# Performance work log

Hardware: AMD Instinct MI355X
Metric: run time of the kernel (lower is better)

## Reference

```python
import jax, jax.numpy as jnp
import numpy as np

B, C, H, W = 16, 4, 64, 64
D_MODEL, D_INNER, D_STATE, D_CONV, DT_RANK = 64, 128, 16, 4, 4


def _mamba_params(key, prefix):
    ks = jax.random.split(key, 6)
    s = lambda k, shape, scale: jax.random.normal(k, shape, jnp.float32) * scale
    return {
        prefix + 'in_proj_w': s(ks[0], (2 * D_INNER, D_MODEL), 0.05),
        prefix + 'conv_w': s(ks[1], (D_INNER, 1, D_CONV), 0.2),
        prefix + 'conv_b': jnp.zeros((D_INNER,), jnp.float32),
        prefix + 'x_proj_w': s(ks[2], (DT_RANK + 2 * D_STATE, D_INNER), 0.05),
        prefix + 'dt_proj_w': s(ks[3], (D_INNER, DT_RANK), 0.1),
        prefix + 'dt_proj_b': s(ks[4], (D_INNER,), 0.1),
        prefix + 'A_log': jnp.log(jnp.broadcast_to(jnp.arange(1, D_STATE + 1, dtype=jnp.float32), (D_INNER, D_STATE))),
        prefix + 'D': jnp.ones((D_INNER,), jnp.float32),
        prefix + 'out_proj_w': s(ks[5], (D_MODEL, D_INNER), 0.05),
    }


def setup_inputs() -> dict:
    key = jax.random.key(0)
    ks = jax.random.split(key, 5)
    inp = {'z_damaged': jax.random.normal(ks[0], (B, C, H, W), jnp.float32)}
    inp['emb_w'] = jax.random.normal(ks[1], (D_MODEL, C), jnp.float32) * 0.1
    inp['emb_b'] = jnp.zeros((D_MODEL,), jnp.float32)
    inp.update(_mamba_params(ks[2], 'm1_'))
    inp.update(_mamba_params(ks[3], 'm2_'))
    inp['ln1_g'] = jnp.ones((D_MODEL,), jnp.float32)
    inp['ln1_b'] = jnp.zeros((D_MODEL,), jnp.float32)
    inp['ln2_g'] = jnp.ones((D_MODEL,), jnp.float32)
    inp['ln2_b'] = jnp.zeros((D_MODEL,), jnp.float32)
    inp['head_w'] = jax.random.normal(ks[4], (C, D_MODEL), jnp.float32) * 0.1
    inp['head_b'] = jnp.zeros((C,), jnp.float32)
    return inp


def _silu(x):
    return x * jax.nn.sigmoid(x)


def _layernorm(x, g, b, eps=1e-5):
    mu = x.mean(-1, keepdims=True)
    var = ((x - mu) ** 2).mean(-1, keepdims=True)
    return (x - mu) * jax.lax.rsqrt(var + eps) * g + b


def _mamba(x, in_proj_w, conv_w, conv_b, x_proj_w, dt_proj_w, dt_proj_b, A_log, Dp, out_proj_w):
    Bb, L, _ = x.shape
    xz = x @ in_proj_w.T                      # [B,L,2*Di]
    u, z = jnp.split(xz, 2, axis=-1)
    # causal depthwise conv over the sequence axis (left-pad K-1)
    uc = jnp.transpose(u, (0, 2, 1))          # [B,Di,L]
    uc = jax.lax.conv_general_dilated(uc, conv_w, (1,), [(D_CONV - 1, 0)],
                                      dimension_numbers=('NCH', 'OIH', 'NCH'),
                                      feature_group_count=D_INNER)
    uc = uc + conv_b[None, :, None]
    u = _silu(jnp.transpose(uc, (0, 2, 1)))   # [B,L,Di]
    x_dbl = u @ x_proj_w.T                    # [B,L,dt_rank+2N]
    dt, Bm, Cm = jnp.split(x_dbl, [DT_RANK, DT_RANK + D_STATE], axis=-1)
    dt = jax.nn.softplus(dt @ dt_proj_w.T + dt_proj_b)   # [B,L,Di]
    A = -jnp.exp(A_log)                       # [Di,N]
    dA = jnp.exp(jnp.einsum('bld,dn->bldn', dt, A))      # [B,L,Di,N]
    dBu = jnp.einsum('bld,bln,bld->bldn', dt, Bm, u)     # [B,L,Di,N]

    def step(h, inp):
        dA_t, dBu_t, C_t = inp
        h = dA_t * h + dBu_t                  # [B,Di,N]
        return h, jnp.einsum('bdn,bn->bd', h, C_t)

    h0 = jnp.zeros((Bb, D_INNER, D_STATE), x.dtype)
    _, ys = jax.lax.scan(step, h0, (jnp.moveaxis(dA, 1, 0), jnp.moveaxis(dBu, 1, 0), jnp.moveaxis(Cm, 1, 0)))
    y = jnp.moveaxis(ys, 0, 1) + u * Dp       # [B,L,Di]
    y = y * _silu(z)
    return y @ out_proj_w.T                   # [B,L,D_MODEL]


def reference(z_damaged, emb_w, emb_b,
              m1_in_proj_w, m1_conv_w, m1_conv_b, m1_x_proj_w, m1_dt_proj_w, m1_dt_proj_b, m1_A_log, m1_D, m1_out_proj_w,
              m2_in_proj_w, m2_conv_w, m2_conv_b, m2_x_proj_w, m2_dt_proj_w, m2_dt_proj_b, m2_A_log, m2_D, m2_out_proj_w,
              ln1_g, ln1_b, ln2_g, ln2_b, head_w, head_b):
    Bz, Cz, Hh, Ww = z_damaged.shape
    zf = jnp.transpose(z_damaged, (0, 2, 3, 1)).reshape(Bz, Hh * Ww, Cz)
    feat = zf @ emb_w.T + emb_b
    feat = _mamba(feat, m1_in_proj_w, m1_conv_w, m1_conv_b, m1_x_proj_w, m1_dt_proj_w, m1_dt_proj_b, m1_A_log, m1_D, m1_out_proj_w)
    feat = _layernorm(feat, ln1_g, ln1_b)
    feat = _mamba(feat, m2_in_proj_w, m2_conv_w, m2_conv_b, m2_x_proj_w, m2_dt_proj_w, m2_dt_proj_b, m2_A_log, m2_D, m2_out_proj_w)
    feat = _layernorm(feat, ln2_g, ln2_b)
    drift = feat @ head_w.T + head_b          # [B,L,C]
    drift = jnp.transpose(drift.reshape(Bz, Hh, Ww, Cz), (0, 3, 1, 2))
    return z_damaged - drift
```

## Files before the change

kernel.cpp:

```cpp
#include <hip/hip_runtime.h>
#include <hip/hip_bf16.h>

#define DEV __device__ __forceinline__

static constexpr int Bn = 16;
static constexpr int Cc = 4;
static constexpr int HW = 4096;
static constexpr int BL = Bn * HW;
static constexpr int DM = 64;
static constexpr int DI = 128;
static constexpr int NS = 16;
static constexpr int NC = 256;
static constexpr int CS = HW / NC;

DEV float sigmoid_f(float x) { return 1.f / (1.f + __expf(-x)); }
DEV float softplus_f(float x) {
    return fmaxf(x, 0.f) + __logf(1.f + __expf(-fabsf(x)));
}
DEV float silu_f(float x) { return x / (1.f + __expf(-x)); }

__global__ __launch_bounds__(256) void k_embed(const float* __restrict__ z,
                                               const float* __restrict__ ew,
                                               const float* __restrict__ eb,
                                               float* __restrict__ feat) {
    int idx = blockIdx.x * 256 + threadIdx.x;
    if (idx >= BL * DM) return;
    int m = idx & 63;
    int bl = idx >> 6;
    int b = bl >> 12;
    int hw = bl & 4095;
    const float* zp = z + (size_t)b * Cc * HW + hw;
    float acc = eb[m];
#pragma unroll
    for (int c = 0; c < 4; ++c) acc += zp[(size_t)c * HW] * ew[m * 4 + c];
    feat[idx] = acc;
}

template <int K, int BN, int TN, int TM>
__global__ __launch_bounds__(256) void k_gemm(const float* __restrict__ in,
                                              const float* __restrict__ W,
                                              float* __restrict__ out,
                                              int Nfull) {
    constexpr int BM = 64;
    constexpr int CT = BN / TN;
    constexpr int RT = BM / TM;
    constexpr int KP = K + 4;
    constexpr int WP = BN + 4;
    __shared__ float As[BM * KP];
    __shared__ float Ws[K * WP];
    int tid = threadIdx.x;
    int n0 = blockIdx.y * BN;
    int row0 = blockIdx.x * BM;
    for (int i = tid; i < BN * (K / 4); i += 256) {
        int c = i / (K / 4);
        int k4 = i - c * (K / 4);
        float4 w = *reinterpret_cast<const float4*>(&W[(size_t)(n0 + c) * K + k4 * 4]);
        Ws[(k4 * 4 + 0) * WP + c] = w.x;
        Ws[(k4 * 4 + 1) * WP + c] = w.y;
        Ws[(k4 * 4 + 2) * WP + c] = w.z;
        Ws[(k4 * 4 + 3) * WP + c] = w.w;
    }
    for (int i = tid; i < BM * (K / 4); i += 256) {
        int r = i / (K / 4);
        int k4 = i - r * (K / 4);
        *reinterpret_cast<float4*>(&As[r * KP + k4 * 4]) =
            *reinterpret_cast<const float4*>(&in[(size_t)(row0 + r) * K + k4 * 4]);
    }
    __syncthreads();
    if (tid < CT * RT) {
        int ty = tid / CT, tx = tid - (tid / CT) * CT;
        int r0 = ty * TM, c0 = tx * TN;
        float acc[TM][TN];
#pragma unroll
        for (int i = 0; i < TM; ++i)
#pragma unroll
            for (int c = 0; c < TN; ++c) acc[i][c] = 0.f;
        for (int k = 0; k < K; k += 4) {
            float4 a[TM];
#pragma unroll
            for (int i = 0; i < TM; ++i)
                a[i] = *reinterpret_cast<const float4*>(&As[(r0 + i) * KP + k]);
            float bv[4][TN];
#pragma unroll
            for (int j = 0; j < 4; ++j)
#pragma unroll
                for (int c = 0; c < TN; ++c) bv[j][c] = Ws[(k + j) * WP + c0 + c];
#pragma unroll
            for (int i = 0; i < TM; ++i)
#pragma unroll
                for (int c = 0; c < TN; ++c)
                    acc[i][c] += a[i].x * bv[0][c] + a[i].y * bv[1][c]
                               + a[i].z * bv[2][c] + a[i].w * bv[3][c];
        }
#pragma unroll
        for (int i = 0; i < TM; ++i) {
            size_t o = (size_t)(row0 + r0 + i) * Nfull + n0 + c0;
            if constexpr (TN == 4) {
                float4 v = {acc[i][0], acc[i][1], acc[i][2], acc[i][3]};
                *reinterpret_cast<float4*>(&out[o]) = v;
            } else {
#pragma unroll
                for (int c = 0; c < TN; ++c) out[o + c] = acc[i][c];
            }
        }
    }
}

__global__ __launch_bounds__(256) void k_xproj(const float* __restrict__ xz,
                                               const float* __restrict__ W,
                                               const float* __restrict__ cw,
                                               const float* __restrict__ cb,
                                               float* __restrict__ xdbl) {
    constexpr int BM = 64, K = 128, BN = 36, TN = 3, TM = 4;
    constexpr int CT = BN / TN;
    constexpr int RT = BM / TM;
    constexpr int KP = K + 4;
    constexpr int WP = BN + 4;
    __shared__ float Xs[(BM + 3) * KP];
    __shared__ float Ws[K * WP];
    int tid = threadIdx.x;
    int row0 = blockIdx.x * BM;
    bool first = (row0 & 4095) == 0;
    for (int i = tid; i < BN * (K / 4); i += 256) {
        int c = i / (K / 4);
        int k4 = i - c * (K / 4);
        float4 w = *reinterpret_cast<const float4*>(&W[(size_t)c * K + k4 * 4]);
        Ws[(k4 * 4 + 0) * WP + c] = w.x;
        Ws[(k4 * 4 + 1) * WP + c] = w.y;
        Ws[(k4 * 4 + 2) * WP + c] = w.z;
        Ws[(k4 * 4 + 3) * WP + c] = w.w;
    }
    for (int i = tid; i < (BM + 3) * (K / 4); i += 256) {
        int r = i / (K / 4);
        int k4 = i - r * (K / 4);
        float4 v = {0, 0, 0, 0};
        if (!first || r >= 3)
            v = *reinterpret_cast<const float4*>(&xz[(size_t)(row0 - 3 + r) * 256 + k4 * 4]);
        *reinterpret_cast<float4*>(&Xs[r * KP + k4 * 4]) = v;
    }
    __syncthreads();
    {
        int rg = tid >> 5;
        int c0 = (tid & 31) * 4;
        float4 wr[4];
#pragma unroll
        for (int j = 0; j < 4; ++j)
            wr[j] = *reinterpret_cast<const float4*>(&cw[(c0 + j) * 4]);
        float4 cb4 = *reinterpret_cast<const float4*>(&cb[c0]);
        int R0 = rg * 8;
        float4 xr[11];
#pragma unroll
        for (int j = 0; j < 11; ++j)
            xr[j] = *reinterpret_cast<const float4*>(&Xs[(R0 + j) * KP + c0]);
        float4 ur[8];
#pragma unroll
        for (int j = 0; j < 8; ++j) {
            float4 acc;
            acc.x = cb4.x + wr[0].x * xr[j].x + wr[0].y * xr[j + 1].x + wr[0].z * xr[j + 2].x + wr[0].w * xr[j + 3].x;
            acc.y = cb4.y + wr[1].x * xr[j].y + wr[1].y * xr[j + 1].y + wr[1].z * xr[j + 2].y + wr[1].w * xr[j + 3].y;
            acc.z = cb4.z + wr[2].x * xr[j].z + wr[2].y * xr[j + 1].z + wr[2].z * xr[j + 2].z + wr[2].w * xr[j + 3].z;
            acc.w = cb4.w + wr[3].x * xr[j].w + wr[3].y * xr[j + 1].w + wr[3].z * xr[j + 2].w + wr[3].w * xr[j + 3].w;
            ur[j].x = silu_f(acc.x);
            ur[j].y = silu_f(acc.y);
            ur[j].z = silu_f(acc.z);
            ur[j].w = silu_f(acc.w);
        }
        __syncthreads();
#pragma unroll
        for (int j = 0; j < 8; ++j)
            *reinterpret_cast<float4*>(&Xs[(R0 + j) * KP + c0]) = ur[j];
    }
    __syncthreads();
    if (tid < CT * RT) {
        int ty = tid / CT, tx = tid - (tid / CT) * CT;
        int r0 = ty * TM, c0 = tx * TN;
        float acc[TM][TN];
#pragma unroll
        for (int i = 0; i < TM; ++i)
#pragma unroll
            for (int c = 0; c < TN; ++c) acc[i][c] = 0.f;
        for (int k = 0; k < K; k += 4) {
            float4 a[TM];
#pragma unroll
            for (int i = 0; i < TM; ++i)
                a[i] = *reinterpret_cast<const float4*>(&Xs[(r0 + i) * KP + k]);
            float bv[4][TN];
#pragma unroll
            for (int j = 0; j < 4; ++j)
#pragma unroll
                for (int c = 0; c < TN; ++c) bv[j][c] = Ws[(k + j) * WP + c0 + c];
#pragma unroll
            for (int i = 0; i < TM; ++i)
#pragma unroll
                for (int c = 0; c < TN; ++c)
                    acc[i][c] += a[i].x * bv[0][c] + a[i].y * bv[1][c]
                               + a[i].z * bv[2][c] + a[i].w * bv[3][c];
        }
#pragma unroll
        for (int i = 0; i < TM; ++i) {
            size_t o = (size_t)(row0 + r0 + i) * BN + c0;
#pragma unroll
            for (int c = 0; c < TN; ++c) xdbl[o + c] = acc[i][c];
        }
    }
}

DEV bool load_a_struct(const float* Alog, int d, float4& a0v, float4& a1v,
                       float4& a2v, float4& a3v, float& a0) {
    const float4* al = reinterpret_cast<const float4*>(Alog + d * NS);
    float4 t0 = al[0], t1 = al[1], t2 = al[2], t3 = al[3];
    a0v.x = -__expf(t0.x); a0v.y = -__expf(t0.y); a0v.z = -__expf(t0.z); a0v.w = -__expf(t0.w);
    a1v.x = -__expf(t1.x); a1v.y = -__expf(t1.y); a1v.z = -__expf(t1.z); a1v.w = -__expf(t1.w);
    a2v.x = -__expf(t2.x); a2v.y = -__expf(t2.y); a2v.z = -__expf(t2.z); a2v.w = -__expf(t2.w);
    a3v.x = -__expf(t3.x); a3v.y = -__expf(t3.y); a3v.z = -__expf(t3.z); a3v.w = -__expf(t3.w);
    a0 = a0v.x;
    float aa[16] = {a0v.x, a0v.y, a0v.z, a0v.w, a1v.x, a1v.y, a1v.z, a1v.w,
                    a2v.x, a2v.y, a2v.z, a2v.w, a3v.x, a3v.y, a3v.z, a3v.w};
    bool fast = true;
#pragma unroll
    for (int n = 0; n < 16; ++n)
        fast = fast && (fabsf(aa[n] - a0 * (float)(n + 1)) <= 1e-4f * (float)(n + 1));
    return fast;
}

#define POWERS(dt, a0, D0, D1, D2, D3)                        \
    {                                                         \
        float E1 = __expf((dt) * (a0));                       \
        float E2 = E1 * E1, E3 = E2 * E1, E4 = E2 * E2;       \
        float E5 = E3 * E2, E6 = E3 * E3, E7 = E4 * E3;       \
        float E8 = E4 * E4, E9 = E5 * E4, E10 = E5 * E5;      \
        float E11 = E6 * E5, E12 = E6 * E6, E13 = E7 * E6;    \
        float E14 = E7 * E7, E15 = E8 * E7, E16 = E8 * E8;    \
        D0 = {E1, E2, E3, E4};                                \
        D1 = {E5, E6, E7, E8};                                \
        D2 = {E9, E10, E11, E12};                             \
        D3 = {E13, E14, E15, E16};                            \
    }

#define UPD4D(H, DA, BV)                          \
    H.x = DA.x * H.x + du * BV.x;                 \
    H.y = DA.y * H.y + du * BV.y;                 \
    H.z = DA.z * H.z + du * BV.z;                 \
    H.w = DA.w * H.w + du * BV.w;

#define UPD4E(H, A, BV)                                  \
    H.x = __expf(dt * A.x) * H.x + du * BV.x;            \
    H.y = __expf(dt * A.y) * H.y + du * BV.y;            \
    H.z = __expf(dt * A.z) * H.z + du * BV.z;            \
    H.w = __expf(dt * A.w) * H.w + du * BV.w;

#define CONV_WARMUP                                                     \
    float x3 = 0.f, x2 = 0.f, x1 = 0.f;                                 \
    if (c != 0) {                                                       \
        size_t wb = ((size_t)b * HW + t0) * 256 + d;                    \
        x3 = xz[wb - 3 * 256];                                          \
        x2 = xz[wb - 2 * 256];                                          \
        x1 = xz[wb - 1 * 256];                                          \
    }

#define CONV_STEP(base)                                                 \
    float xv = xz[(base) * 256 + d];                                    \
    float cacc = cbv + cwv.x * x3 + cwv.y * x2 + cwv.z * x1 + cwv.w * xv; \
    float uu = cacc * sigmoid_f(cacc);                                  \
    x3 = x2; x2 = x1; x1 = xv;

__global__ __launch_bounds__(128, 4) void k_scan1(const float* __restrict__ xz,
                                                  const float* __restrict__ xdbl,
                                                  const float* __restrict__ dpw,
                                                  const float* __restrict__ dpb,
                                                  const float* __restrict__ Alog,
                                                  const float* __restrict__ cw,
                                                  const float* __restrict__ cb,
                                                  float* __restrict__ cS,
                                                  float* __restrict__ cDT) {
    int blk = blockIdx.x;
    int b = blk / NC;
    int c = blk % NC;
    int d = threadIdx.x;
    float4 a0v, a1v, a2v, a3v;
    float a0;
    bool fast = load_a_struct(Alog, d, a0v, a1v, a2v, a3v, a0);
    float4 w = *reinterpret_cast<const float4*>(dpw + d * 4);
    float bb = dpb[d];
    float4 cwv = *reinterpret_cast<const float4*>(cw + d * 4);
    float cbv = cb[d];
    float4 h0 = {0, 0, 0, 0}, h1 = {0, 0, 0, 0}, h2 = {0, 0, 0, 0}, h3 = {0, 0, 0, 0};
    float sdt = 0.f;
    int t0 = c * CS;
    CONV_WARMUP
    if (fast) {
        for (int tt = 0; tt < CS; ++tt) {
            size_t base = (size_t)b * HW + t0 + tt;
            const float4* xd4 = reinterpret_cast<const float4*>(xdbl + base * 36);
            float4 x0 = xd4[0];
            float4 B0 = xd4[1], B1 = xd4[2], B2 = xd4[3], B3 = xd4[4];
            float dt = softplus_f(w.x * x0.x + w.y * x0.y + w.z * x0.z + w.w * x0.w + bb);
            CONV_STEP(base)
            float du = dt * uu;
            sdt += dt;
            float4 D0, D1, D2, D3;
            POWERS(dt, a0, D0, D1, D2, D3)
            UPD4D(h0, D0, B0) UPD4D(h1, D1, B1) UPD4D(h2, D2, B2) UPD4D(h3, D3, B3)
        }
    } else {
        for (int tt = 0; tt < CS; ++tt) {
            size_t base = (size_t)b * HW + t0 + tt;
            const float4* xd4 = reinterpret_cast<const float4*>(xdbl + base * 36);
            float4 x0 = xd4[0];
            float4 B0 = xd4[1], B1 = xd4[2], B2 = xd4[3], B3 = xd4[4];
            float dt = softplus_f(w.x * x0.x + w.y * x0.y + w.z * x0.z + w.w * x0.w + bb);
            CONV_STEP(base)
            float du = dt * uu;
            sdt += dt;
            UPD4E(h0, a0v, B0) UPD4E(h1, a1v, B1) UPD4E(h2, a2v, B2) UPD4E(h3, a3v, B3)
        }
    }
    size_t o = (size_t)blk * DI + d;
    cDT[o] = sdt;
    float4* cs4 = reinterpret_cast<float4*>(cS + o * NS);
    cs4[0] = h0; cs4[1] = h1; cs4[2] = h2; cs4[3] = h3;
}

__global__ __launch_bounds__(256) void k_scan2(float* __restrict__ cS,
                                               const float* __restrict__ cDT,
                                               const float* __restrict__ Alog) {
    int idx = blockIdx.x * 256 + threadIdx.x;
    if (idx >= Bn * DI * NS) return;
    int n = idx & 15;
    int d = (idx >> 4) & 127;
    int b = idx >> 11;
    float a = -__expf(Alog[d * NS + n]);
    float h = 0.f;
    for (int c = 0; c < NC; ++c) {
        size_t o = (size_t)(b * NC + c) * DI + d;
        float s = cS[o * NS + n];
        cS[o * NS + n] = h;
        h = __expf(a * cDT[o]) * h + s;
    }
}

__global__ __launch_bounds__(128, 4) void k_scan3(float* __restrict__ uy,
                                                  const float* __restrict__ xz,
                                                  const float* __restrict__ xdbl,
                                                  const float* __restrict__ dpw,
                                                  const float* __restrict__ dpb,
                                                  const float* __restrict__ Alog,
                                                  const float* __restrict__ Dp,
                                                  const float* __restrict__ cw,
                                                  const float* __restrict__ cb,
                                                  const float* __restrict__ iS) {
    int blk = blockIdx.x;
    int b = blk / NC;
    int c = blk % NC;
    int d = threadIdx.x;
    float4 a0v, a1v, a2v, a3v;
    float a0;
    bool fast = load_a_struct(Alog, d, a0v, a1v, a2v, a3v, a0);
    float4 w = *reinterpret_cast<const float4*>(dpw + d * 4);
    float bb = dpb[d];
    float Dv = Dp[d];
    float4 cwv = *reinterpret_cast<const float4*>(cw + d * 4);
    float cbv = cb[d];
    size_t so = (size_t)blk * DI + d;
    const float4* is4 = reinterpret_cast<const float4*>(iS + so * NS);
    float4 h0 = is4[0], h1 = is4[1], h2 = is4[2], h3 = is4[3];
    int t0 = c * CS;
    CONV_WARMUP
    if (fast) {
        for (int tt = 0; tt < CS; ++tt) {
            size_t base = (size_t)b * HW + t0 + tt;
            const float4* xd4 = reinterpret_cast<const float4*>(xdbl + base * 36);
            float4 x0 = xd4[0];
            float4 B0 = xd4[1], B1 = xd4[2], B2 = xd4[3], B3 = xd4[4];
            float4 C0 = xd4[5], C1 = xd4[6], C2 = xd4[7], C3 = xd4[8];
            float dt = softplus_f(w.x * x0.x + w.y * x0.y + w.z * x0.z + w.w * x0.w + bb);
            CONV_STEP(base)
            float du = dt * uu;
            float4 D0, D1, D2, D3;
            POWERS(dt, a0, D0, D1, D2, D3)
            UPD4D(h0, D0, B0) UPD4D(h1, D1, B1) UPD4D(h2, D2, B2) UPD4D(h3, D3, B3)
            float y = h0.x * C0.x + h0.y * C0.y + h0.z * C0.z + h0.w * C0.w
                    + h1.x * C1.x + h1.y * C1.y + h1.z * C1.z + h1.w * C1.w
                    + h2.x * C2.x + h2.y * C2.y + h2.z * C2.z + h2.w * C2.w
                    + h3.x * C3.x + h3.y * C3.y + h3.z * C3.z + h3.w * C3.w;
            y += uu * Dv;
            float zz = xz[base * 256 + 128 + d];
            y *= zz * sigmoid_f(zz);
            uy[base * DI + d] = y;
        }
    } else {
        for (int tt = 0; tt < CS; ++tt) {
            size_t base = (size_t)b * HW + t0 + tt;
            const float4* xd4 = reinterpret_cast<const float4*>(xdbl + base * 36);
            float4 x0 = xd4[0];
            float4 B0 = xd4[1], B1 = xd4[2], B2 = xd4[3], B3 = xd4[4];
            float4 C0 = xd4[5], C1 = xd4[6], C2 = xd4[7], C3 = xd4[8];
            float dt = softplus_f(w.x * x0.x + w.y * x0.y + w.z * x0.z + w.w * x0.w + bb);
            CONV_STEP(base)
            float du = dt * uu;
            UPD4E(h0, a0v, B0) UPD4E(h1, a1v, B1) UPD4E(h2, a2v, B2) UPD4E(h3, a3v, B3)
            float y = h0.x * C0.x + h0.y * C0.y + h0.z * C0.z + h0.w * C0.w
                    + h1.x * C1.x + h1.y * C1.y + h1.z * C1.z + h1.w * C1.w
                    + h2.x * C2.x + h2.y * C2.y + h2.z * C2.z + h2.w * C2.w
                    + h3.x * C3.x + h3.y * C3.y + h3.z * C3.z + h3.w * C3.w;
            y += uu * Dv;
            float zz = xz[base * 256 + 128 + d];
            y *= zz * sigmoid_f(zz);
            uy[base * DI + d] = y;
        }
    }
}

__global__ __launch_bounds__(256) void k_ln(float* __restrict__ feat,
                                            const float* __restrict__ g,
                                            const float* __restrict__ bta, int R) {
    int lane = threadIdx.x & 63;
    int wv = blockIdx.x * 4 + (threadIdx.x >> 6);
    int stride = gridDim.x * 4;
    for (int row = wv; row < R; row += stride) {
        float x = feat[(size_t)row * 64 + lane];
        float s = x;
#pragma unroll
        for (int off = 32; off; off >>= 1) s += __shfl_xor(s, off, 64);
        float mu = s * (1.f / 64.f);
        float xm = x - mu;
        float v = xm * xm;
#pragma unroll
        for (int off = 32; off; off >>= 1) v += __shfl_xor(v, off, 64);
        float var = v * (1.f / 64.f);
        feat[(size_t)row * 64 + lane] = xm * rsqrtf(var + 1e-5f) * g[lane] + bta[lane];
    }
}

__global__ __launch_bounds__(256) void k_head(const float* __restrict__ feat,
                                              const float* __restrict__ hwt,
                                              const float* __restrict__ hb,
                                              const float* __restrict__ z,
                                              float* __restrict__ out) {
    __shared__ float fl[64 * 65];
    int row0 = blockIdx.x * 64;
    for (int i = threadIdx.x; i < 64 * 64; i += 256) {
        int r = i >> 6;
        int m = i & 63;
        fl[r * 65 + m] = feat[(size_t)(row0 + r) * 64 + m];
    }
    __syncthreads();
    int r = threadIdx.x >> 2;
    int c = threadIdx.x & 3;
    float acc = hb[c];
#pragma unroll
    for (int m = 0; m < 64; ++m) acc += fl[r * 65 + m] * hwt[c * 64 + m];
    int bl = row0 + r;
    int b = bl >> 12;
    int hw = bl & 4095;
    size_t o = ((size_t)b * 4 + c) * HW + hw;
    out[o] = z[o] - acc;
}

static void run_mamba(const float* const* P, float* feat, float* xz, float* u,
                      float* xdbl, float* cS, float* cDT, hipStream_t s) {
    k_gemm<64, 64, 4, 8><<<dim3(BL / 64, 4), 256, 0, s>>>(feat, P[0], xz, 256);
    k_xproj<<<BL / 64, 256, 0, s>>>(xz, P[3], P[1], P[2], xdbl);
    k_scan1<<<Bn * NC, DI, 0, s>>>(xz, xdbl, P[4], P[5], P[6], P[1], P[2], cS, cDT);
    k_scan2<<<(Bn * DI * NS) / 256, 256, 0, s>>>(cS, cDT, P[6]);
    k_scan3<<<Bn * NC, DI, 0, s>>>(u, xz, xdbl, P[4], P[5], P[6], P[7], P[1], P[2], cS);
    k_gemm<128, 64, 4, 8><<<dim3(BL / 64, 1), 256, 0, s>>>(u, P[8], feat, 64);
}

extern "C" void kernel_launch(void* const* d_in, const int* in_sizes, int n_in,
                              void* d_out, int out_size, void* d_ws, size_t ws_size,
                              hipStream_t stream) {
    const float* z = (const float*)d_in[0];
    const float* ew = (const float*)d_in[1];
    const float* eb = (const float*)d_in[2];
    const float* m1[9];
    const float* m2[9];
    for (int i = 0; i < 9; ++i) m1[i] = (const float*)d_in[3 + i];
    for (int i = 0; i < 9; ++i) m2[i] = (const float*)d_in[12 + i];
    const float* ln1g = (const float*)d_in[21];
    const float* ln1b = (const float*)d_in[22];
    const float* ln2g = (const float*)d_in[23];
    const float* ln2b = (const float*)d_in[24];
    const float* hwt = (const float*)d_in[25];
    const float* hb = (const float*)d_in[26];

    float* ws = (float*)d_ws;
    float* feat = ws;
    float* xz = feat + (size_t)BL * 64;
    float* u = xz + (size_t)BL * 256;
    float* xdbl = u + (size_t)BL * 128;
    float* cS = xdbl + (size_t)BL * 36;
    float* cDT = cS + (size_t)Bn * NC * DI * NS;

    k_embed<<<(BL * DM) / 256, 256, 0, stream>>>(z, ew, eb, feat);

    run_mamba(m1, feat, xz, u, xdbl, cS, cDT, stream);
    k_ln<<<4096, 256, 0, stream>>>(feat, ln1g, ln1b, BL);
    run_mamba(m2, feat, xz, u, xdbl, cS, cDT, stream);
    k_ln<<<4096, 256, 0, stream>>>(feat, ln2g, ln2b, BL);

    k_head<<<BL / 64, 256, 0, stream>>>(feat, hwt, hb, z, (float*)d_out);
}
```

Before: 549.3 us.

## Fuse embedding and layernorms into GEMM prologues and head kernel

Removes the separate embed and two layernorm kernels. The embedding is computed directly into the first in_proj GEMM's shared-memory tile, LN1 is applied in the second mamba's in_proj prologue, and LN2 is folded into the head kernel. The GEMMs also switch to a 4x4 register tile using all 256 threads and strided row assignment, with float4 weight loads. This cuts global round trips over the 64-wide feature tensor and several launches. In exchange, LN1 is recomputed by each of the four column blocks of the in_proj GEMM.

```diff
diff --git a/kernel.cpp b/kernel.cpp
--- a/kernel.cpp
+++ b/kernel.cpp
@@ -19,35 +19,24 @@
 }
 DEV float silu_f(float x) { return x / (1.f + __expf(-x)); }
 
-__global__ __launch_bounds__(256) void k_embed(const float* __restrict__ z,
-                                               const float* __restrict__ ew,
-                                               const float* __restrict__ eb,
-                                               float* __restrict__ feat) {
-    int idx = blockIdx.x * 256 + threadIdx.x;
-    if (idx >= BL * DM) return;
-    int m = idx & 63;
-    int bl = idx >> 6;
-    int b = bl >> 12;
-    int hw = bl & 4095;
-    const float* zp = z + (size_t)b * Cc * HW + hw;
-    float acc = eb[m];
-#pragma unroll
-    for (int c = 0; c < 4; ++c) acc += zp[(size_t)c * HW] * ew[m * 4 + c];
-    feat[idx] = acc;
-}
-
-template <int K, int BN, int TN, int TM>
-__global__ __launch_bounds__(256) void k_gemm(const float* __restrict__ in,
-                                              const float* __restrict__ W,
-                                              float* __restrict__ out,
-                                              int Nfull) {
-    constexpr int BM = 64;
+template <int K, int BN, int MODE>
+__global__ __launch_bounds__(256) void k_gemmf(const float* __restrict__ in,
+                                               const float* __restrict__ W,
+                                               float* __restrict__ out,
+                                               int Nfull,
+                                               const float* __restrict__ p0,
+                                               const float* __restrict__ p1,
+                                               const float* __restrict__ p2) {
+    constexpr int BM = 64, TM = 4, TN = 4;
     constexpr int CT = BN / TN;
     constexpr int RT = BM / TM;
     constexpr int KP = K + 4;
     constexpr int WP = BN + 4;
     __shared__ float As[BM * KP];
     __shared__ float Ws[K * WP];
+    __shared__ float GBs[128];
+    __shared__ float4 EW4[64];
+    __shared__ float EBs[64];
     int tid = threadIdx.x;
     int n0 = blockIdx.y * BN;
     int row0 = blockIdx.x * BM;
@@ -60,16 +49,71 @@
         Ws[(k4 * 4 + 2) * WP + c] = w.z;
         Ws[(k4 * 4 + 3) * WP + c] = w.w;
     }
-    for (int i = tid; i < BM * (K / 4); i += 256) {
-        int r = i / (K / 4);
-        int k4 = i - r * (K / 4);
-        *reinterpret_cast<float4*>(&As[r * KP + k4 * 4]) =
-            *reinterpret_cast<const float4*>(&in[(size_t)(row0 + r) * K + k4 * 4]);
+    if constexpr (MODE == 0) {
+        for (int i = tid; i < BM * (K / 4); i += 256) {
+            int r = i / (K / 4);
+            int k4 = i - r * (K / 4);
+            *reinterpret_cast<float4*>(&As[r * KP + k4 * 4]) =
+                *reinterpret_cast<const float4*>(&in[(size_t)(row0 + r) * K + k4 * 4]);
+        }
+    } else if constexpr (MODE == 1) {
+        if (tid < 64) {
+            EW4[tid] = *reinterpret_cast<const float4*>(&p1[tid * 4]);
+            EBs[tid] = p2[tid];
+        }
+        __syncthreads();
+        int r = tid >> 2, q = tid & 3, m0 = q * 16;
+        int grow = row0 + r;
+        int b = grow >> 12, hw = grow & 4095;
+        float zv0 = p0[((size_t)b * 4 + 0) * HW + hw];
+        float zv1 = p0[((size_t)b * 4 + 1) * HW + hw];
+        float zv2 = p0[((size_t)b * 4 + 2) * HW + hw];
+        float zv3 = p0[((size_t)b * 4 + 3) * HW + hw];
+#pragma unroll
+        for (int mi = 0; mi < 16; ++mi) {
+            int m = m0 + mi;
+            float4 e = EW4[m];
+            As[r * KP + m] = EBs[m] + e.x * zv0 + e.y * zv1 + e.z * zv2 + e.w * zv3;
+        }
+    } else {
+        for (int i = tid; i < BM * (K / 4); i += 256) {
+            int r = i / (K / 4);
+            int k4 = i - r * (K / 4);
+            *reinterpret_cast<float4*>(&As[r * KP + k4 * 4]) =
+                *reinterpret_cast<const float4*>(&in[(size_t)(row0 + r) * K + k4 * 4]);
+        }
+        if (tid < 64) {
+            GBs[tid] = p0[tid];
+            GBs[64 + tid] = p1[tid];
+        }
+        __syncthreads();
+        int r = tid >> 2, q = tid & 3, m0 = q * 16;
+        float s = 0.f;
+#pragma unroll
+        for (int mi = 0; mi < 16; ++mi) s += As[r * KP + m0 + mi];
+        s += __shfl_xor(s, 1, 64);
+        s += __shfl_xor(s, 2, 64);
+        float mu = s * (1.f / 64.f);
+        float v = 0.f;
+#pragma unroll
+        for (int mi = 0; mi < 16; ++mi) {
+            float dd = As[r * KP + m0 + mi] - mu;
+            v += dd * dd;
+        }
+        v += __shfl_xor(v, 1, 64);
+        v += __shfl_xor(v, 2, 64);
+        float rs = rsqrtf(v * (1.f / 64.f) + 1e-5f);
+#pragma unroll
+        for (int mi = 0; mi < 16; ++mi) {
+            int m = m0 + mi;
+            float x = As[r * KP + m];
+            As[r * KP + m] = (x - mu) * rs * GBs[m] + GBs[64 + m];
+        }
     }
     __syncthreads();
-    if (tid < CT * RT) {
+    {
         int ty = tid / CT, tx = tid - (tid / CT) * CT;
-        int r0 = ty * TM, c0 = tx * TN;
+        int c0 = tx * TN;
         float acc[TM][TN];
 #pragma unroll
         for (int i = 0; i < TM; ++i)
@@ -79,29 +123,24 @@
             float4 a[TM];
 #pragma unroll
             for (int i = 0; i < TM; ++i)
-                a[i] = *reinterpret_cast<const float4*>(&As[(r0 + i) * KP + k]);
-            float bv[4][TN];
-#pragma unroll
-            for (int j = 0; j < 4; ++j)
-#pragma unroll
-                for (int c = 0; c < TN; ++c) bv[j][c] = Ws[(k + j) * WP + c0 + c];
-#pragma unroll
-            for (int i = 0; i < TM; ++i)
-#pragma unroll
-                for (int c = 0; c < TN; ++c)
-                    acc[i][c] += a[i].x * bv[0][c] + a[i].y * bv[1][c]
-                               + a[i].z * bv[2][c] + a[i].w * bv[3][c];
+                a[i] = *reinterpret_cast<const float4*>(&As[(ty + i * RT) * KP + k]);
+            float4 b0 = *reinterpret_cast<const float4*>(&Ws[(k + 0) * WP + c0]);
+            float4 b1 = *reinterpret_cast<const float4*>(&Ws[(k + 1) * WP + c0]);
+            float4 b2 = *reinterpret_cast<const float4*>(&Ws[(k + 2) * WP + c0]);
+            float4 b3 = *reinterpret_cast<const float4*>(&Ws[(k + 3) * WP + c0]);
+#pragma unroll
+            for (int i = 0; i < TM; ++i) {
+                acc[i][0] += a[i].x * b0.x + a[i].y * b1.x + a[i].z * b2.x + a[i].w * b3.x;
+                acc[i][1] += a[i].x * b0.y + a[i].y * b1.y + a[i].z * b2.y + a[i].w * b3.y;
+                acc[i][2] += a[i].x * b0.z + a[i].y * b1.z + a[i].z * b2.z + a[i].w * b3.z;
+                acc[i][3] += a[i].x * b0.w + a[i].y * b1.w + a[i].z * b2.w + a[i].w * b3.w;
+            }
         }
 #pragma unroll
         for (int i = 0; i < TM; ++i) {
-            size_t o = (size_t)(row0 + r0 + i) * Nfull + n0 + c0;
-            if constexpr (TN == 4) {
-                float4 v = {acc[i][0], acc[i][1], acc[i][2], acc[i][3]};
-                *reinterpret_cast<float4*>(&out[o]) = v;
-            } else {
-#pragma unroll
-                for (int c = 0; c < TN; ++c) out[o + c] = acc[i][c];
-            }
+            size_t o = (size_t)(row0 + ty + i * RT) * Nfull + n0 + c0;
+            float4 v = {acc[i][0], acc[i][1], acc[i][2], acc[i][3]};
+            *reinterpret_cast<float4*>(&out[o]) = v;
         }
     }
 }
@@ -173,7 +212,7 @@
     __syncthreads();
     if (tid < CT * RT) {
         int ty = tid / CT, tx = tid - (tid / CT) * CT;
-        int r0 = ty * TM, c0 = tx * TN;
+        int c0 = tx * TN;
         float acc[TM][TN];
 #pragma unroll
         for (int i = 0; i < TM; ++i)
@@ -183,7 +222,7 @@
             float4 a[TM];
 #pragma unroll
             for (int i = 0; i < TM; ++i)
-                a[i] = *reinterpret_cast<const float4*>(&Xs[(r0 + i) * KP + k]);
+                a[i] = *reinterpret_cast<const float4*>(&Xs[(ty + i * RT) * KP + k]);
             float bv[4][TN];
 #pragma unroll
             for (int j = 0; j < 4; ++j)
@@ -198,7 +237,7 @@
         }
 #pragma unroll
         for (int i = 0; i < TM; ++i) {
-            size_t o = (size_t)(row0 + r0 + i) * BN + c0;
+            size_t o = (size_t)(row0 + ty + i * RT) * BN + c0;
 #pragma unroll
             for (int c = 0; c < TN; ++c) xdbl[o + c] = acc[i][c];
         }
@@ -411,30 +450,11 @@
     }
 }
 
-__global__ __launch_bounds__(256) void k_ln(float* __restrict__ feat,
-                                            const float* __restrict__ g,
-                                            const float* __restrict__ bta, int R) {
-    int lane = threadIdx.x & 63;
-    int wv = blockIdx.x * 4 + (threadIdx.x >> 6);
-    int stride = gridDim.x * 4;
-    for (int row = wv; row < R; row += stride) {
-        float x = feat[(size_t)row * 64 + lane];
-        float s = x;
-#pragma unroll
-        for (int off = 32; off; off >>= 1) s += __shfl_xor(s, off, 64);
-        float mu = s * (1.f / 64.f);
-        float xm = x - mu;
-        float v = xm * xm;
-#pragma unroll
-        for (int off = 32; off; off >>= 1) v += __shfl_xor(v, off, 64);
-        float var = v * (1.f / 64.f);
-        feat[(size_t)row * 64 + lane] = xm * rsqrtf(var + 1e-5f) * g[lane] + bta[lane];
-    }
-}
-
 __global__ __launch_bounds__(256) void k_head(const float* __restrict__ feat,
                                               const float* __restrict__ hwt,
                                               const float* __restrict__ hb,
+                                              const float* __restrict__ g,
+                                              const float* __restrict__ bta,
                                               const float* __restrict__ z,
                                               float* __restrict__ out) {
     __shared__ float fl[64 * 65];
@@ -447,6 +467,29 @@
     __syncthreads();
     int r = threadIdx.x >> 2;
     int c = threadIdx.x & 3;
+    int m0 = c * 16;
+    float s = 0.f;
+#pragma unroll
+    for (int mi = 0; mi < 16; ++mi) s += fl[r * 65 + m0 + mi];
+    s += __shfl_xor(s, 1, 64);
+    s += __shfl_xor(s, 2, 64);
+    float mu = s * (1.f / 64.f);
+    float v = 0.f;
+#pragma unroll
+    for (int mi = 0; mi < 16; ++mi) {
+        float dd = fl[r * 65 + m0 + mi] - mu;
+        v += dd * dd;
+    }
+    v += __shfl_xor(v, 1, 64);
+    v += __shfl_xor(v, 2, 64);
+    float rs = rsqrtf(v * (1.f / 64.f) + 1e-5f);
+#pragma unroll
+    for (int mi = 0; mi < 16; ++mi) {
+        int m = m0 + mi;
+        float x = fl[r * 65 + m];
+        fl[r * 65 + m] = (x - mu) * rs * g[m] + bta[m];
+    }
+    __syncthreads();
     float acc = hb[c];
 #pragma unroll
     for (int m = 0; m < 64; ++m) acc += fl[r * 65 + m] * hwt[c * 64 + m];
@@ -457,14 +500,18 @@
     out[o] = z[o] - acc;
 }
 
-static void run_mamba(const float* const* P, float* feat, float* xz, float* u,
+template <int MODE>
+static void run_mamba(const float* const* P, const float* src0, const float* src1,
+                      const float* src2, float* feat, float* xz, float* u,
                       float* xdbl, float* cS, float* cDT, hipStream_t s) {
-    k_gemm<64, 64, 4, 8><<<dim3(BL / 64, 4), 256, 0, s>>>(feat, P[0], xz, 256);
+    k_gemmf<64, 64, MODE><<<dim3(BL / 64, 4), 256, 0, s>>>(feat, P[0], xz, 256,
+                                                           src0, src1, src2);
     k_xproj<<<BL / 64, 256, 0, s>>>(xz, P[3], P[1], P[2], xdbl);
     k_scan1<<<Bn * NC, DI, 0, s>>>(xz, xdbl, P[4], P[5], P[6], P[1], P[2], cS, cDT);
     k_scan2<<<(Bn * DI * NS) / 256, 256, 0, s>>>(cS, cDT, P[6]);
     k_scan3<<<Bn * NC, DI, 0, s>>>(u, xz, xdbl, P[4], P[5], P[6], P[7], P[1], P[2], cS);
-    k_gemm<128, 64, 4, 8><<<dim3(BL / 64, 1), 256, 0, s>>>(u, P[8], feat, 64);
+    k_gemmf<128, 64, 0><<<dim3(BL / 64, 1), 256, 0, s>>>(u, P[8], feat, 64,
+                                                         nullptr, nullptr, nullptr);
 }
 
 extern "C" void kernel_launch(void* const* d_in, const int* in_sizes, int n_in,
@@ -492,12 +539,7 @@
     float* cS = xdbl + (size_t)BL * 36;
     float* cDT = cS + (size_t)Bn * NC * DI * NS;
 
-    k_embed<<<(BL * DM) / 256, 256, 0, stream>>>(z, ew, eb, feat);
-
-    run_mamba(m1, feat, xz, u, xdbl, cS, cDT, stream);
-    k_ln<<<4096, 256, 0, stream>>>(feat, ln1g, ln1b, BL);
-    run_mamba(m2, feat, xz, u, xdbl, cS, cDT, stream);
-    k_ln<<<4096, 256, 0, stream>>>(feat, ln2g, ln2b, BL);
-
-    k_head<<<BL / 64, 256, 0, stream>>>(feat, hwt, hb, z, (float*)d_out);
-}
+    run_mamba<1>(m1, z, ew, eb, feat, xz, u, xdbl, cS, cDT, stream);
+    run_mamba<2>(m2, ln1g, ln1b, nullptr, feat, xz, u, xdbl, cS, cDT, stream);
+    k_head<<<BL / 64, 256, 0, stream>>>(feat, hwt, hb, ln2g, ln2b, z, (float*)d_out);
+}
```

Result: slower. 565.0 us (+2.9%).

## Retile GEMM to use all threads and fuse final layernorm into head

Applied to the files above, without the earlier changes.

The generic GEMM now uses 4x4 register tiles with interleaved rows, so all 256 threads compute (previously only 128 did with 8x4 tiles), and the B-operand is read from shared memory as float4. The weight-staging loops and the x-projection row mapping are reordered to change shared-memory store and read bank patterns. The second layernorm is fused into the head kernel, computed on the shared-memory tile, which removes one full read/write pass over the feature tensor and a kernel launch. The trade-off is more per-thread shared-memory traffic in the head kernel and an extra barrier.

```diff
diff --git a/kernel.cpp b/kernel.cpp
--- a/kernel.cpp
+++ b/kernel.cpp
@@ -36,12 +36,33 @@
     feat[idx] = acc;
 }
 
-template <int K, int BN, int TN, int TM>
+__global__ __launch_bounds__(256) void k_ln(float* __restrict__ feat,
+                                            const float* __restrict__ g,
+                                            const float* __restrict__ bta, int R) {
+    int lane = threadIdx.x & 63;
+    int wv = blockIdx.x * 4 + (threadIdx.x >> 6);
+    int stride = gridDim.x * 4;
+    for (int row = wv; row < R; row += stride) {
+        float x = feat[(size_t)row * 64 + lane];
+        float s = x;
+#pragma unroll
+        for (int off = 32; off; off >>= 1) s += __shfl_xor(s, off, 64);
+        float mu = s * (1.f / 64.f);
+        float xm = x - mu;
+        float v = xm * xm;
+#pragma unroll
+        for (int off = 32; off; off >>= 1) v += __shfl_xor(v, off, 64);
+        float var = v * (1.f / 64.f);
+        feat[(size_t)row * 64 + lane] = xm * rsqrtf(var + 1e-5f) * g[lane] + bta[lane];
+    }
+}
+
+template <int K, int BN>
 __global__ __launch_bounds__(256) void k_gemm(const float* __restrict__ in,
                                               const float* __restrict__ W,
                                               float* __restrict__ out,
                                               int Nfull) {
-    constexpr int BM = 64;
+    constexpr int BM = 64, TM = 4, TN = 4;
     constexpr int CT = BN / TN;
     constexpr int RT = BM / TM;
     constexpr int KP = K + 4;
@@ -52,8 +73,8 @@
     int n0 = blockIdx.y * BN;
     int row0 = blockIdx.x * BM;
     for (int i = tid; i < BN * (K / 4); i += 256) {
-        int c = i / (K / 4);
-        int k4 = i - c * (K / 4);
+        int k4 = i / BN;
+        int c = i - k4 * BN;
         float4 w = *reinterpret_cast<const float4*>(&W[(size_t)(n0 + c) * K + k4 * 4]);
         Ws[(k4 * 4 + 0) * WP + c] = w.x;
         Ws[(k4 * 4 + 1) * WP + c] = w.y;
@@ -67,42 +88,35 @@
             *reinterpret_cast<const float4*>(&in[(size_t)(row0 + r) * K + k4 * 4]);
     }
     __syncthreads();
-    if (tid < CT * RT) {
-        int ty = tid / CT, tx = tid - (tid / CT) * CT;
-        int r0 = ty * TM, c0 = tx * TN;
-        float acc[TM][TN];
+    int ty = tid / CT, tx = tid - (tid / CT) * CT;
+    int c0 = tx * TN;
+    float acc[TM][TN];
+#pragma unroll
+    for (int i = 0; i < TM; ++i)
+#pragma unroll
+        for (int c = 0; c < TN; ++c) acc[i][c] = 0.f;
+    for (int k = 0; k < K; k += 4) {
+        float4 a[TM];
 #pragma unroll
         for (int i = 0; i < TM; ++i)
-#pragma unroll
-            for (int c = 0; c < TN; ++c) acc[i][c] = 0.f;
-        for (int k = 0; k < K; k += 4) {
-            float4 a[TM];
-#pragma unroll
-            for (int i = 0; i < TM; ++i)
-                a[i] = *reinterpret_cast<const float4*>(&As[(r0 + i) * KP + k]);
-            float bv[4][TN];
-#pragma unroll
-            for (int j = 0; j < 4; ++j)
-#pragma unroll
-                for (int c = 0; c < TN; ++c) bv[j][c] = Ws[(k + j) * WP + c0 + c];
-#pragma unroll
-            for (int i = 0; i < TM; ++i)
-#pragma unroll
-                for (int c = 0; c < TN; ++c)
-                    acc[i][c] += a[i].x * bv[0][c] + a[i].y * bv[1][c]
-                               + a[i].z * bv[2][c] + a[i].w * bv[3][c];
-        }
+            a[i] = *reinterpret_cast<const float4*>(&As[(ty + i * RT) * KP + k]);
+        float4 b0 = *reinterpret_cast<const float4*>(&Ws[(k + 0) * WP + c0]);
+        float4 b1 = *reinterpret_cast<const float4*>(&Ws[(k + 1) * WP + c0]);
+        float4 b2 = *reinterpret_cast<const float4*>(&Ws[(k + 2) * WP + c0]);
+        float4 b3 = *reinterpret_cast<const float4*>(&Ws[(k + 3) * WP + c0]);
 #pragma unroll
         for (int i = 0; i < TM; ++i) {
-            size_t o = (size_t)(row0 + r0 + i) * Nfull + n0 + c0;
-            if constexpr (TN == 4) {
-                float4 v = {acc[i][0], acc[i][1], acc[i][2], acc[i][3]};
-                *reinterpret_cast<float4*>(&out[o]) = v;
-            } else {
-#pragma unroll
-                for (int c = 0; c < TN; ++c) out[o + c] = acc[i][c];
-            }
-        }
+            acc[i][0] += a[i].x * b0.x + a[i].y * b1.x + a[i].z * b2.x + a[i].w * b3.x;
+            acc[i][1] += a[i].x * b0.y + a[i].y * b1.y + a[i].z * b2.y + a[i].w * b3.y;
+            acc[i][2] += a[i].x * b0.z + a[i].y * b1.z + a[i].z * b2.z + a[i].w * b3.z;
+            acc[i][3] += a[i].x * b0.w + a[i].y * b1.w + a[i].z * b2.w + a[i].w * b3.w;
+        }
+    }
+#pragma unroll
+    for (int i = 0; i < TM; ++i) {
+        size_t o = (size_t)(row0 + ty + i * RT) * Nfull + n0 + c0;
+        float4 v = {acc[i][0], acc[i][1], acc[i][2], acc[i][3]};
+        *reinterpret_cast<float4*>(&out[o]) = v;
     }
 }
 
@@ -122,8 +136,8 @@
     int row0 = blockIdx.x * BM;
     bool first = (row0 & 4095) == 0;
     for (int i = tid; i < BN * (K / 4); i += 256) {
-        int c = i / (K / 4);
-        int k4 = i - c * (K / 4);
+        int k4 = i / BN;
+        int c = i - k4 * BN;
         float4 w = *reinterpret_cast<const float4*>(&W[(size_t)c * K + k4 * 4]);
         Ws[(k4 * 4 + 0) * WP + c] = w.x;
         Ws[(k4 * 4 + 1) * WP + c] = w.y;
@@ -173,7 +187,7 @@
     __syncthreads();
     if (tid < CT * RT) {
         int ty = tid / CT, tx = tid - (tid / CT) * CT;
-        int r0 = ty * TM, c0 = tx * TN;
+        int c0 = tx * TN;
         float acc[TM][TN];
 #pragma unroll
         for (int i = 0; i < TM; ++i)
@@ -183,7 +197,7 @@
             float4 a[TM];
 #pragma unroll
             for (int i = 0; i < TM; ++i)
-                a[i] = *reinterpret_cast<const float4*>(&Xs[(r0 + i) * KP + k]);
+                a[i] = *reinterpret_cast<const float4*>(&Xs[(ty + i * RT) * KP + k]);
             float bv[4][TN];
 #pragma unroll
             for (int j = 0; j < 4; ++j)
@@ -198,7 +212,7 @@
         }
 #pragma unroll
         for (int i = 0; i < TM; ++i) {
-            size_t o = (size_t)(row0 + r0 + i) * BN + c0;
+            size_t o = (size_t)(row0 + ty + i * RT) * BN + c0;
 #pragma unroll
             for (int c = 0; c < TN; ++c) xdbl[o + c] = acc[i][c];
         }
@@ -411,30 +425,11 @@
     }
 }
 
-__global__ __launch_bounds__(256) void k_ln(float* __restrict__ feat,
-                                            const float* __restrict__ g,
-                                            const float* __restrict__ bta, int R) {
-    int lane = threadIdx.x & 63;
-    int wv = blockIdx.x * 4 + (threadIdx.x >> 6);
-    int stride = gridDim.x * 4;
-    for (int row = wv; row < R; row += stride) {
-        float x = feat[(size_t)row * 64 + lane];
-        float s = x;
-#pragma unroll
-        for (int off = 32; off; off >>= 1) s += __shfl_xor(s, off, 64);
-        float mu = s * (1.f / 64.f);
-        float xm = x - mu;
-        float v = xm * xm;
-#pragma unroll
-        for (int off = 32; off; off >>= 1) v += __shfl_xor(v, off, 64);
-        float var = v * (1.f / 64.f);
-        feat[(size_t)row * 64 + lane] = xm * rsqrtf(var + 1e-5f) * g[lane] + bta[lane];
-    }
-}
-
 __global__ __launch_bounds__(256) void k_head(const float* __restrict__ feat,
                                               const float* __restrict__ hwt,
                                               const float* __restrict__ hb,
+                                              const float* __restrict__ g,
+                                              const float* __restrict__ bta,
                                               const float* __restrict__ z,
                                               float* __restrict__ out) {
     __shared__ float fl[64 * 65];
@@ -447,6 +442,29 @@
     __syncthreads();
     int r = threadIdx.x >> 2;
     int c = threadIdx.x & 3;
+    int m0 = c * 16;
+    float s = 0.f;
+#pragma unroll
+    for (int mi = 0; mi < 16; ++mi) s += fl[r * 65 + m0 + mi];
+    s += __shfl_xor(s, 1, 64);
+    s += __shfl_xor(s, 2, 64);
+    float mu = s * (1.f / 64.f);
+    float v = 0.f;
+#pragma unroll
+    for (int mi = 0; mi < 16; ++mi) {
+        float dd = fl[r * 65 + m0 + mi] - mu;
+        v += dd * dd;
+    }
+    v += __shfl_xor(v, 1, 64);
+    v += __shfl_xor(v, 2, 64);
+    float rs = rsqrtf(v * (1.f / 64.f) + 1e-5f);
+#pragma unroll
+    for (int mi = 0; mi < 16; ++mi) {
+        int m = m0 + mi;
+        float x = fl[r * 65 + m];
+        fl[r * 65 + m] = (x - mu) * rs * g[m] + bta[m];
+    }
+    __syncthreads();
     float acc = hb[c];
 #pragma unroll
     for (int m = 0; m < 64; ++m) acc += fl[r * 65 + m] * hwt[c * 64 + m];
@@ -459,12 +477,12 @@
 
 static void run_mamba(const float* const* P, float* feat, float* xz, float* u,
                       float* xdbl, float* cS, float* cDT, hipStream_t s) {
-    k_gemm<64, 64, 4, 8><<<dim3(BL / 64, 4), 256, 0, s>>>(feat, P[0], xz, 256);
+    k_gemm<64, 64><<<dim3(BL / 64, 4), 256, 0, s>>>(feat, P[0], xz, 256);
     k_xproj<<<BL / 64, 256, 0, s>>>(xz, P[3], P[1], P[2], xdbl);
     k_scan1<<<Bn * NC, DI, 0, s>>>(xz, xdbl, P[4], P[5], P[6], P[1], P[2], cS, cDT);
     k_scan2<<<(Bn * DI * NS) / 256, 256, 0, s>>>(cS, cDT, P[6]);
     k_scan3<<<Bn * NC, DI, 0, s>>>(u, xz, xdbl, P[4], P[5], P[6], P[7], P[1], P[2], cS);
-    k_gemm<128, 64, 4, 8><<<dim3(BL / 64, 1), 256, 0, s>>>(u, P[8], feat, 64);
+    k_gemm<128, 64><<<dim3(BL / 64, 1), 256, 0, s>>>(u, P[8], feat, 64);
 }
 
 extern "C" void kernel_launch(void* const* d_in, const int* in_sizes, int n_in,
@@ -493,11 +511,8 @@
     float* cDT = cS + (size_t)Bn * NC * DI * NS;
 
     k_embed<<<(BL * DM) / 256, 256, 0, stream>>>(z, ew, eb, feat);
-
     run_mamba(m1, feat, xz, u, xdbl, cS, cDT, stream);
     k_ln<<<4096, 256, 0, stream>>>(feat, ln1g, ln1b, BL);
     run_mamba(m2, feat, xz, u, xdbl, cS, cDT, stream);
-    k_ln<<<4096, 256, 0, stream>>>(feat, ln2g, ln2b, BL);
-
-    k_head<<<BL / 64, 256, 0, stream>>>(feat, hwt, hb, z, (float*)d_out);
-}
+    k_head<<<BL / 64, 256, 0, stream>>>(feat, hwt, hb, ln2g, ln2b, z, (float*)d_out);
+}
```

Result: no change. 558.3 us (+1.6%).
